# Kernel tuning notes

Measured on AMD Instinct MI355X. Metric: run time of the kernel, lower is better.

## Reference

```python
import jax, jax.numpy as jnp
import numpy as np
import math

B, N, E, H, MLP_H = 4, 1024, 768, 12, 1536
D = E // H
EPS = 1e-6


def clayernorm(x, gamma, beta):
    # x: [..., E, 2]
    real, imag = x[..., 0], x[..., 1]
    mag = jnp.sqrt(real * real + imag * imag + EPS)
    mean = jnp.mean(mag, axis=-1, keepdims=True)
    var = jnp.mean((mag - mean) ** 2, axis=-1, keepdims=True)
    scale = ((mag - mean) / jnp.sqrt(var + EPS)) / (mag + EPS)
    out_r = gamma[:, 0] * (real * scale) + beta[:, 0]
    out_i = gamma[:, 1] * (imag * scale) + beta[:, 1]
    return jnp.stack([out_r, out_i], axis=-1)


def clinear(x, wr, wi, br, bi):
    # x: [..., in, 2]; wr/wi: [out, in]
    xr, xi = x[..., 0], x[..., 1]
    out_r = xr @ wr.T - xi @ wi.T + br
    out_i = xr @ wi.T + xi @ wr.T + bi
    return jnp.stack([out_r, out_i], axis=-1)


def cgelu(x):
    return jnp.stack([jax.nn.gelu(x[..., 0], approximate=False),
                      jax.nn.gelu(x[..., 1], approximate=False)], axis=-1)


def setup_inputs() -> dict:
    key = jax.random.key(0)
    ks = jax.random.split(key, 8)
    std_qkv = math.sqrt(2.0 / (E + 3 * E))
    std_proj = math.sqrt(2.0 / (E + E))
    std_m1 = math.sqrt(2.0 / (E + MLP_H))
    std_m2 = math.sqrt(2.0 / (MLP_H + E))
    return {
        "x": jax.random.normal(ks[0], (B, N, 2 * E), dtype=jnp.float32),
        "g1": jnp.ones((E, 2), jnp.float32), "b1": jnp.zeros((E, 2), jnp.float32),
        "g2": jnp.ones((E, 2), jnp.float32), "b2": jnp.zeros((E, 2), jnp.float32),
        "qkv_wr": std_qkv * jax.random.normal(ks[1], (3 * E, E), jnp.float32),
        "qkv_wi": std_qkv * jax.random.normal(ks[2], (3 * E, E), jnp.float32),
        "qkv_br": jnp.zeros((3 * E,), jnp.float32), "qkv_bi": jnp.zeros((3 * E,), jnp.float32),
        "proj_wr": std_proj * jax.random.normal(ks[3], (E, E), jnp.float32),
        "proj_wi": std_proj * jax.random.normal(ks[4], (E, E), jnp.float32),
        "proj_br": jnp.zeros((E,), jnp.float32), "proj_bi": jnp.zeros((E,), jnp.float32),
        "m1_wr": std_m1 * jax.random.normal(ks[5], (MLP_H, E), jnp.float32),
        "m1_wi": std_m1 * jax.random.normal(ks[6], (MLP_H, E), jnp.float32),
        "m1_br": jnp.zeros((MLP_H,), jnp.float32), "m1_bi": jnp.zeros((MLP_H,), jnp.float32),
        "m2_wr": std_m2 * jax.random.normal(ks[7], (E, MLP_H), jnp.float32),
        "m2_wi": std_m2 * jax.random.normal(jax.random.fold_in(key, 9), (E, MLP_H), jnp.float32),
        "m2_br": jnp.zeros((E,), jnp.float32), "m2_bi": jnp.zeros((E,), jnp.float32),
    }


def _forward(x, g1, b1, g2, b2, qkv_wr, qkv_wi, qkv_br, qkv_bi,
             proj_wr, proj_wi, proj_br, proj_bi,
             m1_wr, m1_wi, m1_br, m1_bi, m2_wr, m2_wi, m2_br, m2_bi):
    xc = x.reshape(B, N, E, 2)
    xn = clayernorm(xc, g1, b1)
    qkv = clinear(xn, qkv_wr, qkv_wi, qkv_br, qkv_bi)      # [B,N,3E,2]
    qkv = qkv.reshape(B, N, 3, H, D, 2).transpose(2, 0, 3, 1, 4, 5)  # [3,B,H,N,D,2]
    q, k, v = qkv[0], qkv[1], qkv[2]
    qr, qi = q[..., 0], q[..., 1]
    kr, ki = k[..., 0], k[..., 1]
    attn_r = jnp.einsum('bhqd,bhkd->bhqk', qr, kr) + jnp.einsum('bhqd,bhkd->bhqk', qi, ki)
    attn_i = jnp.einsum('bhqd,bhkd->bhqk', qr, ki) - jnp.einsum('bhqd,bhkd->bhqk', qi, kr)
    mag = jnp.sqrt(attn_r * attn_r + attn_i * attn_i + 1e-8) / math.sqrt(D)
    w = jax.nn.softmax(mag, axis=-1)
    out_r = jnp.einsum('bhqk,bhkd->bhqd', w, v[..., 0])
    out_i = jnp.einsum('bhqk,bhkd->bhqd', w, v[..., 1])
    attn_out = jnp.stack([out_r, out_i], axis=-1)           # [B,H,N,D,2]
    attn_out = attn_out.transpose(0, 2, 1, 3, 4).reshape(B, N, E, 2)
    attn_out = clinear(attn_out, proj_wr, proj_wi, proj_br, proj_bi)
    xc = xc + attn_out
    xn2 = clayernorm(xc, g2, b2)
    h = clinear(xn2, m1_wr, m1_wi, m1_br, m1_bi)
    h = cgelu(h)
    mlp_out = clinear(h, m2_wr, m2_wi, m2_br, m2_bi)
    xc = xc + mlp_out
    return xc.reshape(B, N, 2 * E)


def reference(x, g1, b1, g2, b2, qkv_wr, qkv_wi, qkv_br, qkv_bi,
              proj_wr, proj_wi, proj_br, proj_bi,
              m1_wr, m1_wi, m1_br, m1_bi, m2_wr, m2_wi, m2_br, m2_bi):
    return _forward(x, g1, b1, g2, b2, qkv_wr, qkv_wi, qkv_br, qkv_bi,
                    proj_wr, proj_wi, proj_br, proj_bi,
                    m1_wr, m1_wi, m1_br, m1_bi, m2_wr, m2_wi, m2_br, m2_bi)
```

## Files before the change

### kernel.cpp

```cpp
#include <hip/hip_runtime.h>
#include <math.h>

#define BB 4
#define NN 1024
#define EE 768
#define HH 12
#define DD 64
#define MLPH 1536
#define RR (BB*NN)
#define SZH ((size_t)48*1024*64)

constexpr float EPS = 1e-6f;

typedef __bf16 bf16_t;
typedef bf16_t bf16x8 __attribute__((ext_vector_type(8)));
typedef bf16_t bf16x4 __attribute__((ext_vector_type(4)));
typedef float  f32x4  __attribute__((ext_vector_type(4)));
typedef unsigned short us8 __attribute__((ext_vector_type(8)));

__device__ __forceinline__ float gelu_exact(float x){
  return 0.5f * x * (1.0f + erff(x * 0.70710678118654752440f));
}

__device__ __forceinline__ bf16x8 negv(bf16x8 v){
  us8 u = __builtin_bit_cast(us8, v);
  u ^= (unsigned short)0x8000;
  return __builtin_bit_cast(bf16x8, u);
}

__device__ __forceinline__ void cvtstore(bf16_t* hp, bf16_t* lp, f32x4 v){
  bf16x4 h, l;
  #pragma unroll
  for (int i=0;i<4;i++){
    float f = v[i];
    bf16_t hb = (bf16_t)f;
    h[i] = hb;
    l[i] = (bf16_t)(f - (float)hb);
  }
  *(bf16x4*)hp = h;
  *(bf16x4*)lp = l;
}

__global__ __launch_bounds__(256) void cln_kernel(
    const float* __restrict__ inI,
    const float* __restrict__ inR, const float* __restrict__ inIm,
    const float* __restrict__ gamma, const float* __restrict__ beta,
    float* __restrict__ outR, float* __restrict__ outI, int mode)
{
  int row = blockIdx.x;
  int t = threadIdx.x;
  __shared__ float sbuf[4];
  float vr[3], vi[3], mg[3];
  #pragma unroll
  for (int j=0;j<3;j++){
    int e = t + 256*j;
    float a, b;
    if (mode == 0){
      a = inI[(size_t)row*(2*EE) + 2*e];
      b = inI[(size_t)row*(2*EE) + 2*e + 1];
    } else {
      a = inR[(size_t)row*EE + e];
      b = inIm[(size_t)row*EE + e];
    }
    vr[j]=a; vi[j]=b;
    mg[j] = sqrtf(a*a + b*b + EPS);
  }
  int lane = t & 63, wv = t >> 6;
  float s = mg[0]+mg[1]+mg[2];
  #pragma unroll
  for (int o=32;o>0;o>>=1) s += __shfl_down(s, o, 64);
  if (lane==0) sbuf[wv] = s;
  __syncthreads();
  float mean = (sbuf[0]+sbuf[1]+sbuf[2]+sbuf[3]) * (1.0f/EE);
  __syncthreads();
  float v = 0.f;
  #pragma unroll
  for (int j=0;j<3;j++){ float d = mg[j]-mean; v += d*d; }
  #pragma unroll
  for (int o=32;o>0;o>>=1) v += __shfl_down(v, o, 64);
  if (lane==0) sbuf[wv] = v;
  __syncthreads();
  float var = (sbuf[0]+sbuf[1]+sbuf[2]+sbuf[3]) * (1.0f/EE);
  float inv = 1.0f / sqrtf(var + EPS);
  #pragma unroll
  for (int j=0;j<3;j++){
    int e = t + 256*j;
    float scale = ((mg[j]-mean) * inv) / (mg[j] + EPS);
    outR[(size_t)row*EE + e] = gamma[2*e]   * (vr[j]*scale) + beta[2*e];
    outI[(size_t)row*EE + e] = gamma[2*e+1] * (vi[j]*scale) + beta[2*e+1];
  }
}

template<int ACT, int RES_MODE, int OUT_MODE>
__global__ __launch_bounds__(256) void cgemm_mfma(
    const float* __restrict__ xr, const float* __restrict__ xi,
    const float* __restrict__ wr, const float* __restrict__ wi,
    const float* __restrict__ br_, const float* __restrict__ bi_,
    const float* __restrict__ resr, const float* __restrict__ resi,
    float* __restrict__ outr, float* __restrict__ outi,
    bf16_t* __restrict__ qsplit,
    int K, int OUT)
{
  __shared__ bf16_t Arh[128][40], Arl[128][40], Aih[128][40], Ail[128][40];
  __shared__ bf16_t Brh[64][40],  Brl[64][40],  Bih[64][40],  Bil[64][40];

  const int tid = threadIdx.x;
  const int rowBase = blockIdx.y * 128, colBase = blockIdx.x * 64;

  const int sr = tid >> 3;
  const int sc = (tid & 7) * 4;

  const int wid = tid >> 6, lane = tid & 63;
  const int wr0 = (wid >> 1) * 64, wc0 = (wid & 1) * 32;
  const int fr = lane & 15, fq = lane >> 4;

  f32x4 accR[4][2], accI[4][2];
  #pragma unroll
  for (int mi=0;mi<4;mi++)
    #pragma unroll
    for (int ni=0;ni<2;ni++){ accR[mi][ni] = (f32x4)0.f; accI[mi][ni] = (f32x4)0.f; }

  f32x4 pAr[4], pAi[4], pBr[2], pBi[2];

  auto LOAD = [&](int k0){
    #pragma unroll
    for (int it=0; it<4; it++){
      const size_t ro = (size_t)(rowBase + sr + it*32)*K + k0 + sc;
      pAr[it] = *(const f32x4*)(xr + ro);
      pAi[it] = *(const f32x4*)(xi + ro);
    }
    #pragma unroll
    for (int it=0; it<2; it++){
      const size_t ro = (size_t)(colBase + sr + it*32)*K + k0 + sc;
      pBr[it] = *(const f32x4*)(wr + ro);
      pBi[it] = *(const f32x4*)(wi + ro);
    }
  };

  LOAD(0);

  for (int k0 = 0; k0 < K; k0 += 32){
    __syncthreads();
    #pragma unroll
    for (int it=0; it<4; it++){
      int r = sr + it*32;
      cvtstore(&Arh[r][sc], &Arl[r][sc], pAr[it]);
      cvtstore(&Aih[r][sc], &Ail[r][sc], pAi[it]);
    }
    #pragma unroll
    for (int it=0; it<2; it++){
      int r = sr + it*32;
      cvtstore(&Brh[r][sc], &Brl[r][sc], pBr[it]);
      cvtstore(&Bih[r][sc], &Bil[r][sc], pBi[it]);
    }
    __syncthreads();
    if (k0 + 32 < K) LOAD(k0 + 32);

    bf16x8 brh[2], brl[2], bih[2], bil[2];
    #pragma unroll
    for (int ni=0; ni<2; ni++){
      int c = wc0 + ni*16 + fr;
      brh[ni] = *(const bf16x8*)&Brh[c][fq*8];
      brl[ni] = *(const bf16x8*)&Brl[c][fq*8];
      bih[ni] = *(const bf16x8*)&Bih[c][fq*8];
      bil[ni] = *(const bf16x8*)&Bil[c][fq*8];
    }
    #pragma unroll
    for (int mi=0; mi<4; mi++){
      int r = wr0 + mi*16 + fr;
      bf16x8 arh = *(const bf16x8*)&Arh[r][fq*8];
      bf16x8 arl = *(const bf16x8*)&Arl[r][fq*8];
      bf16x8 aih = *(const bf16x8*)&Aih[r][fq*8];
      bf16x8 ail = *(const bf16x8*)&Ail[r][fq*8];
      bf16x8 nih = negv(aih), nil_ = negv(ail);
      #pragma unroll
      for (int ni=0; ni<2; ni++){
        f32x4 cR = accR[mi][ni], cI = accI[mi][ni];
        cR = __builtin_amdgcn_mfma_f32_16x16x32_bf16(arh, brh[ni], cR, 0,0,0);
        cR = __builtin_amdgcn_mfma_f32_16x16x32_bf16(arh, brl[ni], cR, 0,0,0);
        cR = __builtin_amdgcn_mfma_f32_16x16x32_bf16(arl, brh[ni], cR, 0,0,0);
        cR = __builtin_amdgcn_mfma_f32_16x16x32_bf16(nih, bih[ni], cR, 0,0,0);
        cR = __builtin_amdgcn_mfma_f32_16x16x32_bf16(nih, bil[ni], cR, 0,0,0);
        cR = __builtin_amdgcn_mfma_f32_16x16x32_bf16(nil_, bih[ni], cR, 0,0,0);
        cI = __builtin_amdgcn_mfma_f32_16x16x32_bf16(arh, bih[ni], cI, 0,0,0);
        cI = __builtin_amdgcn_mfma_f32_16x16x32_bf16(arh, bil[ni], cI, 0,0,0);
        cI = __builtin_amdgcn_mfma_f32_16x16x32_bf16(arl, bih[ni], cI, 0,0,0);
        cI = __builtin_amdgcn_mfma_f32_16x16x32_bf16(aih, brh[ni], cI, 0,0,0);
        cI = __builtin_amdgcn_mfma_f32_16x16x32_bf16(aih, brl[ni], cI, 0,0,0);
        cI = __builtin_amdgcn_mfma_f32_16x16x32_bf16(ail, brh[ni], cI, 0,0,0);
        accR[mi][ni] = cR; accI[mi][ni] = cI;
      }
    }
  }

  #pragma unroll
  for (int mi=0; mi<4; mi++){
    #pragma unroll
    for (int ni=0; ni<2; ni++){
      #pragma unroll
      for (int j=0; j<4; j++){
        int r = rowBase + wr0 + mi*16 + fq*4 + j;
        int c = colBase + wc0 + ni*16 + fr;
        float oR = accR[mi][ni][j] + br_[c];
        float oI = accI[mi][ni][j] + bi_[c];
        if (ACT == 1){ oR = gelu_exact(oR); oI = gelu_exact(oI); }
        if (RES_MODE == 1){
          oR += resr[(size_t)r*OUT + c];
          oI += resi[(size_t)r*OUT + c];
        } else if (RES_MODE == 2){
          oR += resr[(size_t)r*(2*OUT) + 2*c];
          oI += resr[(size_t)r*(2*OUT) + 2*c + 1];
        }
        if (OUT_MODE == 0){
          outr[(size_t)r*OUT + c] = oR;
          outi[(size_t)r*OUT + c] = oI;
        } else if (OUT_MODE == 1){
          outr[(size_t)r*(2*OUT) + 2*c]     = oR;
          outr[(size_t)r*(2*OUT) + 2*c + 1] = oI;
        } else {
          int part = c / EE; int win = c - part*EE;
          int hh = win >> 6, dd = win & 63;
          int bq = r >> 10, nq = r & 1023;
          int bhh = bq*HH + hh;
          size_t idx = (part < 2) ? (((size_t)bhh*NN + nq)*DD + dd)
                                  : (((size_t)bhh*DD + dd)*NN + nq);
          bf16_t* bas = qsplit + (size_t)part*4*SZH;
          bf16_t hR = (bf16_t)oR; bf16_t lR2 = (bf16_t)(oR - (float)hR);
          bf16_t hI = (bf16_t)oI; bf16_t lI2 = (bf16_t)(oI - (float)hI);
          bas[idx]         = hR;
          bas[SZH + idx]   = lR2;
          bas[2*SZH + idx] = hI;
          bas[3*SZH + idx] = lI2;
        }
      }
    }
  }
}

__global__ __launch_bounds__(256) void cattn_mfma(
    const bf16_t* __restrict__ qs,
    float* __restrict__ aor, float* __restrict__ aoi)
{
  __shared__ bf16_t Krh[32][72], Krl[32][72], Kih[32][72], Kil[32][72];
  __shared__ bf16_t Vrh[64][40], Vrl[64][40], Vih[64][40], Vil[64][40];
  __shared__ bf16_t Pl[4][16][40];

  const int tid = threadIdx.x;
  const int lane = tid & 63, wid = tid >> 6;
  const int fr = lane & 15, fq = lane >> 4;
  const int qt = blockIdx.x, bh = blockIdx.y;
  const int b = bh / HH, h = bh - b*HH;

  const bf16_t* Qb = qs;
  const bf16_t* Kb = qs + 4*SZH;
  const bf16_t* Vb = qs + 8*SZH;

  const int qrow = qt*64 + wid*16 + fr;
  bf16x8 q_rh[2], q_rl[2], q_ih[2], q_il[2], nq_ih[2], nq_il[2];
  #pragma unroll
  for (int c=0;c<2;c++){
    size_t o = ((size_t)bh*NN + qrow)*DD + c*32 + fq*8;
    q_rh[c] = *(const bf16x8*)(Qb + 0*SZH + o);
    q_rl[c] = *(const bf16x8*)(Qb + 1*SZH + o);
    q_ih[c] = *(const bf16x8*)(Qb + 2*SZH + o);
    q_il[c] = *(const bf16x8*)(Qb + 3*SZH + o);
    nq_ih[c] = negv(q_ih[c]);
    nq_il[c] = negv(q_il[c]);
  }

  f32x4 accOr[4], accOi[4];
  #pragma unroll
  for (int df=0;df<4;df++){ accOr[df] = (f32x4)0.f; accOi[df] = (f32x4)0.f; }
  float m[4] = {0.f,0.f,0.f,0.f}, l[4] = {0.f,0.f,0.f,0.f};

  const int skr = tid >> 3, skc = (tid & 7) * 8;
  const int svr = tid >> 2, svc = (tid & 3) * 8;

  for (int kt = 0; kt < NN/32; kt++){
    __syncthreads();
    {
      size_t kb = ((size_t)bh*NN + kt*32 + skr)*DD + skc;
      *(bf16x8*)&Krh[skr][skc] = *(const bf16x8*)(Kb + 0*SZH + kb);
      *(bf16x8*)&Krl[skr][skc] = *(const bf16x8*)(Kb + 1*SZH + kb);
      *(bf16x8*)&Kih[skr][skc] = *(const bf16x8*)(Kb + 2*SZH + kb);
      *(bf16x8*)&Kil[skr][skc] = *(const bf16x8*)(Kb + 3*SZH + kb);
      size_t vb = ((size_t)bh*DD + svr)*NN + kt*32 + svc;
      *(bf16x8*)&Vrh[svr][svc] = *(const bf16x8*)(Vb + 0*SZH + vb);
      *(bf16x8*)&Vrl[svr][svc] = *(const bf16x8*)(Vb + 1*SZH + vb);
      *(bf16x8*)&Vih[svr][svc] = *(const bf16x8*)(Vb + 2*SZH + vb);
      *(bf16x8*)&Vil[svr][svc] = *(const bf16x8*)(Vb + 3*SZH + vb);
    }
    __syncthreads();

    f32x4 sr[2], si[2];
    #pragma unroll
    for (int f=0; f<2; f++){
      f32x4 r = (f32x4)0.f, im = (f32x4)0.f;
      #pragma unroll
      for (int c=0; c<2; c++){
        const int kr_ = f*16 + fr, co = c*32 + fq*8;
        bf16x8 krh = *(const bf16x8*)&Krh[kr_][co];
        bf16x8 krl = *(const bf16x8*)&Krl[kr_][co];
        bf16x8 kih = *(const bf16x8*)&Kih[kr_][co];
        bf16x8 kil = *(const bf16x8*)&Kil[kr_][co];
        r = __builtin_amdgcn_mfma_f32_16x16x32_bf16(q_rh[c], krh, r, 0,0,0);
        r = __builtin_amdgcn_mfma_f32_16x16x32_bf16(q_rh[c], krl, r, 0,0,0);
        r = __builtin_amdgcn_mfma_f32_16x16x32_bf16(q_rl[c], krh, r, 0,0,0);
        r = __builtin_amdgcn_mfma_f32_16x16x32_bf16(q_ih[c], kih, r, 0,0,0);
        r = __builtin_amdgcn_mfma_f32_16x16x32_bf16(q_ih[c], kil, r, 0,0,0);
        r = __builtin_amdgcn_mfma_f32_16x16x32_bf16(q_il[c], kih, r, 0,0,0);
        im = __builtin_amdgcn_mfma_f32_16x16x32_bf16(q_rh[c], kih, im, 0,0,0);
        im = __builtin_amdgcn_mfma_f32_16x16x32_bf16(q_rh[c], kil, im, 0,0,0);
        im = __builtin_amdgcn_mfma_f32_16x16x32_bf16(q_rl[c], kih, im, 0,0,0);
        im = __builtin_amdgcn_mfma_f32_16x16x32_bf16(nq_ih[c], krh, im, 0,0,0);
        im = __builtin_amdgcn_mfma_f32_16x16x32_bf16(nq_ih[c], krl, im, 0,0,0);
        im = __builtin_amdgcn_mfma_f32_16x16x32_bf16(nq_il[c], krh, im, 0,0,0);
      }
      sr[f] = r; si[f] = im;
    }

    float mg[2][4];
    #pragma unroll
    for (int f=0; f<2; f++)
      #pragma unroll
      for (int j=0; j<4; j++){
        float a = sr[f][j], c2 = si[f][j];
        mg[f][j] = sqrtf(fmaf(a,a, fmaf(c2,c2, 1e-8f))) * 0.125f;
      }
    float al[4];
    #pragma unroll
    for (int j=0; j<4; j++){
      float mx = fmaxf(mg[0][j], mg[1][j]);
      mx = fmaxf(mx, __shfl_xor(mx, 1, 64));
      mx = fmaxf(mx, __shfl_xor(mx, 2, 64));
      mx = fmaxf(mx, __shfl_xor(mx, 4, 64));
      mx = fmaxf(mx, __shfl_xor(mx, 8, 64));
      float nm = fmaxf(m[j], mx);
      al[j] = __expf(m[j] - nm);
      m[j] = nm;
    }
    unsigned pk[4]; float psum[4];
    #pragma unroll
    for (int j=0; j<4; j++){
      float p0 = __expf(mg[0][j] - m[j]);
      float p1 = __expf(mg[1][j] - m[j]);
      bf16_t b0 = (bf16_t)p0, b1 = (bf16_t)p1;
      pk[j] = (unsigned)__builtin_bit_cast(unsigned short, b0)
            | ((unsigned)__builtin_bit_cast(unsigned short, b1) << 16);
      psum[j] = (float)b0 + (float)b1;
    }
    #pragma unroll
    for (int j=0; j<4; j++){
      float s = psum[j];
      s += __shfl_xor(s, 1, 64);
      s += __shfl_xor(s, 2, 64);
      s += __shfl_xor(s, 4, 64);
      s += __shfl_xor(s, 8, 64);
      l[j] = l[j]*al[j] + s;
      #pragma unroll
      for (int df=0; df<4; df++){ accOr[df][j] *= al[j]; accOi[df][j] *= al[j]; }
    }
    #pragma unroll
    for (int j=0; j<4; j++){
      unsigned partner = (unsigned)__shfl_xor((int)pk[j], 1, 64);
      unsigned word; int kcol;
      if ((fr & 1) == 0){
        word = (pk[j] & 0xFFFFu) | (partner << 16);
        kcol = fr;
      } else {
        word = (partner >> 16) | (pk[j] & 0xFFFF0000u);
        kcol = 15 + fr;
      }
      int q = fq*4 + j;
      *(unsigned*)&Pl[wid][q][kcol] = word;
    }
    __syncthreads();

    bf16x8 pa = *(const bf16x8*)&Pl[wid][fr][fq*8];
    #pragma unroll
    for (int df=0; df<4; df++){
      const int dr = df*16 + fr, co = fq*8;
      bf16x8 vrh = *(const bf16x8*)&Vrh[dr][co];
      bf16x8 vrl = *(const bf16x8*)&Vrl[dr][co];
      bf16x8 vih = *(const bf16x8*)&Vih[dr][co];
      bf16x8 vil = *(const bf16x8*)&Vil[dr][co];
      f32x4 cr = accOr[df], ci = accOi[df];
      cr = __builtin_amdgcn_mfma_f32_16x16x32_bf16(pa, vrh, cr, 0,0,0);
      cr = __builtin_amdgcn_mfma_f32_16x16x32_bf16(pa, vrl, cr, 0,0,0);
      ci = __builtin_amdgcn_mfma_f32_16x16x32_bf16(pa, vih, ci, 0,0,0);
      ci = __builtin_amdgcn_mfma_f32_16x16x32_bf16(pa, vil, ci, 0,0,0);
      accOr[df] = cr; accOi[df] = ci;
    }
  }

  #pragma unroll
  for (int j=0; j<4; j++){
    float invl = 1.0f / l[j];
    size_t r = (size_t)b*NN + qt*64 + wid*16 + fq*4 + j;
    #pragma unroll
    for (int df=0; df<4; df++){
      int col = h*DD + df*16 + fr;
      aor[r*EE + col] = accOr[df][j] * invl;
      aoi[r*EE + col] = accOi[df][j] * invl;
    }
  }
}

extern "C" void kernel_launch(void* const* d_in, const int* in_sizes, int n_in,
                              void* d_out, int out_size, void* d_ws, size_t ws_size,
                              hipStream_t stream) {
  const float* x       = (const float*)d_in[0];
  const float* g1      = (const float*)d_in[1];
  const float* b1      = (const float*)d_in[2];
  const float* g2      = (const float*)d_in[3];
  const float* b2      = (const float*)d_in[4];
  const float* qkv_wr  = (const float*)d_in[5];
  const float* qkv_wi  = (const float*)d_in[6];
  const float* qkv_br  = (const float*)d_in[7];
  const float* qkv_bi  = (const float*)d_in[8];
  const float* proj_wr = (const float*)d_in[9];
  const float* proj_wi = (const float*)d_in[10];
  const float* proj_br = (const float*)d_in[11];
  const float* proj_bi = (const float*)d_in[12];
  const float* m1_wr   = (const float*)d_in[13];
  const float* m1_wi   = (const float*)d_in[14];
  const float* m1_br   = (const float*)d_in[15];
  const float* m1_bi   = (const float*)d_in[16];
  const float* m2_wr   = (const float*)d_in[17];
  const float* m2_wi   = (const float*)d_in[18];
  const float* m2_br   = (const float*)d_in[19];
  const float* m2_bi   = (const float*)d_in[20];

  float* ws = (float*)d_ws;
  const size_t RE = (size_t)RR * EE;
  float* xn_r  = ws;            float* xn_i  = ws + RE;
  float* ao_r  = ws;            float* ao_i  = ws + RE;
  bf16_t* qsplit = (bf16_t*)(ws + 2*RE);
  float* xn2_r = ws + 2*RE;     float* xn2_i = ws + 3*RE;
  float* h_r   = ws + 4*RE;     float* h_i   = ws + 6*RE;
  float* x1_r  = ws + 8*RE;     float* x1_i  = ws + 9*RE;

  cln_kernel<<<RR, 256, 0, stream>>>(x, nullptr, nullptr, g1, b1, xn_r, xn_i, 0);
  cgemm_mfma<0,0,2><<<dim3(36,32), 256, 0, stream>>>(
      xn_r, xn_i, qkv_wr, qkv_wi, qkv_br, qkv_bi,
      nullptr, nullptr, nullptr, nullptr, qsplit, EE, 3*EE);
  cattn_mfma<<<dim3(16,48), 256, 0, stream>>>(qsplit, ao_r, ao_i);
  cgemm_mfma<0,2,0><<<dim3(12,32), 256, 0, stream>>>(
      ao_r, ao_i, proj_wr, proj_wi, proj_br, proj_bi,
      x, nullptr, x1_r, x1_i, nullptr, EE, EE);
  cln_kernel<<<RR, 256, 0, stream>>>(nullptr, x1_r, x1_i, g2, b2, xn2_r, xn2_i, 1);
  cgemm_mfma<1,0,0><<<dim3(24,32), 256, 0, stream>>>(
      xn2_r, xn2_i, m1_wr, m1_wi, m1_br, m1_bi,
      nullptr, nullptr, h_r, h_i, nullptr, EE, MLPH);
  cgemm_mfma<0,1,1><<<dim3(12,32), 256, 0, stream>>>(
      h_r, h_i, m2_wr, m2_wi, m2_br, m2_bi,
      x1_r, x1_i, (float*)d_out, nullptr, nullptr, MLPH, EE);
}
```

Before: 903.3 us.

## Pre-split activations into tiled bf16 hi/lo panels and use 32x32 MFMA GEMM

```diff
diff --git a/kernel.cpp b/kernel.cpp
--- a/kernel.cpp
+++ b/kernel.cpp
@@ -16,7 +16,11 @@
 typedef bf16_t bf16x8 __attribute__((ext_vector_type(8)));
 typedef bf16_t bf16x4 __attribute__((ext_vector_type(4)));
 typedef float  f32x4  __attribute__((ext_vector_type(4)));
+typedef float  f32x16 __attribute__((ext_vector_type(16)));
 typedef unsigned short us8 __attribute__((ext_vector_type(8)));
+
+#define MFMA32 __builtin_amdgcn_mfma_f32_32x32x16_bf16
+#define MFMA16 __builtin_amdgcn_mfma_f32_16x16x32_bf16
 
 __device__ __forceinline__ float gelu_exact(float x){
   return 0.5f * x * (1.0f + erff(x * 0.70710678118654752440f));
@@ -26,6 +30,10 @@
   us8 u = __builtin_bit_cast(us8, v);
   u ^= (unsigned short)0x8000;
   return __builtin_bit_cast(bf16x8, u);
+}
+
+__device__ __forceinline__ void split2(float f, bf16_t& h, bf16_t& l){
+  h = (bf16_t)f; l = (bf16_t)(f - (float)h);
 }
 
 __device__ __forceinline__ void cvtstore(bf16_t* hp, bf16_t* lp, f32x4 v){
@@ -41,12 +49,23 @@
   *(bf16x4*)lp = l;
 }
 
+__device__ __forceinline__ void gload_lds16(const bf16_t* g, bf16_t* l){
+  __builtin_amdgcn_global_load_lds(
+      (const __attribute__((address_space(1))) void*)g,
+      (__attribute__((address_space(3))) void*)l, 16, 0, 0);
+}
+
+__device__ __forceinline__ size_t tiled_ad(int r, int c, int Ko){
+  return (((size_t)(r>>4)*Ko + (c>>3))*16 + (r&15))*8 + (c&7);
+}
+
 __global__ __launch_bounds__(256) void cln_kernel(
     const float* __restrict__ inI,
     const float* __restrict__ inR, const float* __restrict__ inIm,
     const float* __restrict__ gamma, const float* __restrict__ beta,
-    float* __restrict__ outR, float* __restrict__ outI, int mode)
+    bf16_t* __restrict__ out4, int mode)
 {
+  const size_t PS = (size_t)RR*EE;
   int row = blockIdx.x;
   int t = threadIdx.x;
   __shared__ float sbuf[4];
@@ -86,123 +105,138 @@
   for (int j=0;j<3;j++){
     int e = t + 256*j;
     float scale = ((mg[j]-mean) * inv) / (mg[j] + EPS);
-    outR[(size_t)row*EE + e] = gamma[2*e]   * (vr[j]*scale) + beta[2*e];
-    outI[(size_t)row*EE + e] = gamma[2*e+1] * (vi[j]*scale) + beta[2*e+1];
+    float oR = gamma[2*e]   * (vr[j]*scale) + beta[2*e];
+    float oI = gamma[2*e+1] * (vi[j]*scale) + beta[2*e+1];
+    bf16_t hR,lR,hI,lI;
+    split2(oR,hR,lR); split2(oI,hI,lI);
+    size_t ad = tiled_ad(row, e, 96);
+    out4[ad]        = hR;
+    out4[PS + ad]   = lR;
+    out4[2*PS + ad] = hI;
+    out4[3*PS + ad] = lI;
   }
 }
 
 template<int ACT, int RES_MODE, int OUT_MODE>
-__global__ __launch_bounds__(256) void cgemm_mfma(
-    const float* __restrict__ xr, const float* __restrict__ xi,
+__global__ __launch_bounds__(256, 2) void cgemm_v2(
+    const bf16_t* __restrict__ a4,
     const float* __restrict__ wr, const float* __restrict__ wi,
     const float* __restrict__ br_, const float* __restrict__ bi_,
     const float* __restrict__ resr, const float* __restrict__ resi,
     float* __restrict__ outr, float* __restrict__ outi,
-    bf16_t* __restrict__ qsplit,
+    bf16_t* __restrict__ osplit,
     int K, int OUT)
 {
-  __shared__ bf16_t Arh[128][40], Arl[128][40], Aih[128][40], Ail[128][40];
-  __shared__ bf16_t Brh[64][40],  Brl[64][40],  Bih[64][40],  Bil[64][40];
+  __shared__ bf16_t Al[16384];
+  __shared__ bf16_t Bl[16384];
 
   const int tid = threadIdx.x;
-  const int rowBase = blockIdx.y * 128, colBase = blockIdx.x * 64;
-
-  const int sr = tid >> 3;
-  const int sc = (tid & 7) * 4;
-
   const int wid = tid >> 6, lane = tid & 63;
-  const int wr0 = (wid >> 1) * 64, wc0 = (wid & 1) * 32;
-  const int fr = lane & 15, fq = lane >> 4;
-
-  f32x4 accR[4][2], accI[4][2];
-  #pragma unroll
-  for (int mi=0;mi<4;mi++)
-    #pragma unroll
-    for (int ni=0;ni<2;ni++){ accR[mi][ni] = (f32x4)0.f; accI[mi][ni] = (f32x4)0.f; }
-
-  f32x4 pAr[4], pAi[4], pBr[2], pBi[2];
-
-  auto LOAD = [&](int k0){
+  const int rowBase = blockIdx.y * 128, colBase = blockIdx.x * 128;
+  const int Ko = K >> 3;
+  const size_t AS = (size_t)RR * K;
+
+  const int b_so = (tid >> 4) & 3;
+  const int b_se = (tid & 1) * 4;
+  const int b_r0 = ((tid & 15) >> 1) + 8*wid;
+
+  const int fr2 = lane & 31, fq2 = lane >> 5;
+  const int wr0 = (wid >> 1) * 64, wc0 = (wid & 1) * 64;
+
+  f32x16 accR[2][2], accI[2][2];
+  #pragma unroll
+  for (int mi=0;mi<2;mi++)
+    #pragma unroll
+    for (int ni=0;ni<2;ni++){ accR[mi][ni] = (f32x16)0.f; accI[mi][ni] = (f32x16)0.f; }
+
+  f32x4 pBr[4], pBi[4];
+  auto LOADB = [&](int k0){
     #pragma unroll
     for (int it=0; it<4; it++){
-      const size_t ro = (size_t)(rowBase + sr + it*32)*K + k0 + sc;
-      pAr[it] = *(const f32x4*)(xr + ro);
-      pAi[it] = *(const f32x4*)(xi + ro);
-    }
-    #pragma unroll
-    for (int it=0; it<2; it++){
-      const size_t ro = (size_t)(colBase + sr + it*32)*K + k0 + sc;
+      size_t ro = (size_t)(colBase + b_r0 + it*32)*K + k0 + b_so*8 + b_se;
       pBr[it] = *(const f32x4*)(wr + ro);
       pBi[it] = *(const f32x4*)(wi + ro);
     }
   };
-
-  LOAD(0);
+  LOADB(0);
 
   for (int k0 = 0; k0 < K; k0 += 32){
+    const int o0 = k0 >> 3;
     __syncthreads();
     #pragma unroll
     for (int it=0; it<4; it++){
-      int r = sr + it*32;
-      cvtstore(&Arh[r][sc], &Arl[r][sc], pAr[it]);
-      cvtstore(&Aih[r][sc], &Ail[r][sc], pAi[it]);
-    }
-    #pragma unroll
-    for (int it=0; it<2; it++){
-      int r = sr + it*32;
-      cvtstore(&Brh[r][sc], &Brl[r][sc], pBr[it]);
-      cvtstore(&Bih[r][sc], &Bil[r][sc], pBi[it]);
+      int r = b_r0 + it*32;
+      int off = ((r>>4)*4 + b_so)*128 + (r&15)*8 + b_se;
+      cvtstore(&Bl[off],       &Bl[4096+off],  pBr[it]);
+      cvtstore(&Bl[8192+off],  &Bl[12288+off], pBi[it]);
+    }
+    #pragma unroll
+    for (int q=0; q<4; q++){
+      #pragma unroll
+      for (int s2=0; s2<2; s2++){
+        int pi = wid*2 + s2;
+        const bf16_t* g = a4 + (size_t)q*AS
+            + ((size_t)(blockIdx.y*8 + pi)*Ko + o0)*128 + lane*8;
+        gload_lds16(g, &Al[q*4096 + pi*512]);
+      }
     }
     __syncthreads();
-    if (k0 + 32 < K) LOAD(k0 + 32);
-
-    bf16x8 brh[2], brl[2], bih[2], bil[2];
+    if (k0 + 32 < K) LOADB(k0 + 32);
+
+    #pragma unroll
+    for (int ks=0; ks<2; ks++){
+      bf16x8 brh[2], brl[2], bih[2], bil[2];
+      #pragma unroll
+      for (int ni=0; ni<2; ni++){
+        int panelB = (wid&1)*4 + ni*2 + (fr2>>4);
+        int off = ((panelB*4 + ks*2 + fq2)*16 + (fr2&15))*8;
+        brh[ni] = *(const bf16x8*)&Bl[off];
+        brl[ni] = *(const bf16x8*)&Bl[4096+off];
+        bih[ni] = *(const bf16x8*)&Bl[8192+off];
+        bil[ni] = *(const bf16x8*)&Bl[12288+off];
+      }
+      #pragma unroll
+      for (int mi=0; mi<2; mi++){
+        int panelA = (wid>>1)*4 + mi*2 + (fr2>>4);
+        int off = ((panelA*4 + ks*2 + fq2)*16 + (fr2&15))*8;
+        bf16x8 arh = *(const bf16x8*)&Al[off];
+        bf16x8 arl = *(const bf16x8*)&Al[4096+off];
+        bf16x8 aih = *(const bf16x8*)&Al[8192+off];
+        bf16x8 ail = *(const bf16x8*)&Al[12288+off];
+        bf16x8 nih = negv(aih), nil_ = negv(ail);
+        #pragma unroll
+        for (int ni=0; ni<2; ni++){
+          f32x16 cR = accR[mi][ni], cI = accI[mi][ni];
+          cR = MFMA32(arh,  brh[ni], cR, 0,0,0);
+          cR = MFMA32(arh,  brl[ni], cR, 0,0,0);
+          cR = MFMA32(arl,  brh[ni], cR, 0,0,0);
+          cR = MFMA32(nih,  bih[ni], cR, 0,0,0);
+          cR = MFMA32(nih,  bil[ni], cR, 0,0,0);
+          cR = MFMA32(nil_, bih[ni], cR, 0,0,0);
+          cI = MFMA32(arh,  bih[ni], cI, 0,0,0);
+          cI = MFMA32(arh,  bil[ni], cI, 0,0,0);
+          cI = MFMA32(arl,  bih[ni], cI, 0,0,0);
+          cI = MFMA32(aih,  brh[ni], cI, 0,0,0);
+          cI = MFMA32(aih,  brl[ni], cI, 0,0,0);
+          cI = MFMA32(ail,  brh[ni], cI, 0,0,0);
+          accR[mi][ni] = cR; accI[mi][ni] = cI;
+        }
+      }
+    }
+  }
+
+  const size_t OS = (size_t)RR * OUT;
+  #pragma unroll
+  for (int mi=0; mi<2; mi++){
     #pragma unroll
     for (int ni=0; ni<2; ni++){
-      int c = wc0 + ni*16 + fr;
-      brh[ni] = *(const bf16x8*)&Brh[c][fq*8];
-      brl[ni] = *(const bf16x8*)&Brl[c][fq*8];
-      bih[ni] = *(const bf16x8*)&Bih[c][fq*8];
-      bil[ni] = *(const bf16x8*)&Bil[c][fq*8];
-    }
-    #pragma unroll
-    for (int mi=0; mi<4; mi++){
-      int r = wr0 + mi*16 + fr;
-      bf16x8 arh = *(const bf16x8*)&Arh[r][fq*8];
-      bf16x8 arl = *(const bf16x8*)&Arl[r][fq*8];
-      bf16x8 aih = *(const bf16x8*)&Aih[r][fq*8];
-      bf16x8 ail = *(const bf16x8*)&Ail[r][fq*8];
-      bf16x8 nih = negv(aih), nil_ = negv(ail);
-      #pragma unroll
-      for (int ni=0; ni<2; ni++){
-        f32x4 cR = accR[mi][ni], cI = accI[mi][ni];
-        cR = __builtin_amdgcn_mfma_f32_16x16x32_bf16(arh, brh[ni], cR, 0,0,0);
-        cR = __builtin_amdgcn_mfma_f32_16x16x32_bf16(arh, brl[ni], cR, 0,0,0);
-        cR = __builtin_amdgcn_mfma_f32_16x16x32_bf16(arl, brh[ni], cR, 0,0,0);
-        cR = __builtin_amdgcn_mfma_f32_16x16x32_bf16(nih, bih[ni], cR, 0,0,0);
-        cR = __builtin_amdgcn_mfma_f32_16x16x32_bf16(nih, bil[ni], cR, 0,0,0);
-        cR = __builtin_amdgcn_mfma_f32_16x16x32_bf16(nil_, bih[ni], cR, 0,0,0);
-        cI = __builtin_amdgcn_mfma_f32_16x16x32_bf16(arh, bih[ni], cI, 0,0,0);
-        cI = __builtin_amdgcn_mfma_f32_16x16x32_bf16(arh, bil[ni], cI, 0,0,0);
-        cI = __builtin_amdgcn_mfma_f32_16x16x32_bf16(arl, bih[ni], cI, 0,0,0);
-        cI = __builtin_amdgcn_mfma_f32_16x16x32_bf16(aih, brh[ni], cI, 0,0,0);
-        cI = __builtin_amdgcn_mfma_f32_16x16x32_bf16(aih, brl[ni], cI, 0,0,0);
-        cI = __builtin_amdgcn_mfma_f32_16x16x32_bf16(ail, brh[ni], cI, 0,0,0);
-        accR[mi][ni] = cR; accI[mi][ni] = cI;
-      }
-    }
-  }
-
-  #pragma unroll
-  for (int mi=0; mi<4; mi++){
-    #pragma unroll
-    for (int ni=0; ni<2; ni++){
-      #pragma unroll
-      for (int j=0; j<4; j++){
-        int r = rowBase + wr0 + mi*16 + fq*4 + j;
-        int c = colBase + wc0 + ni*16 + fr;
-        float oR = accR[mi][ni][j] + br_[c];
-        float oI = accI[mi][ni][j] + bi_[c];
+      int c = colBase + wc0 + ni*32 + fr2;
+      float bR = br_[c], bI = bi_[c];
+      #pragma unroll
+      for (int j=0; j<16; j++){
+        int r = rowBase + wr0 + mi*32 + (j&3) + 8*(j>>2) + 4*fq2;
+        float oR = accR[mi][ni][j] + bR;
+        float oI = accI[mi][ni][j] + bI;
         if (ACT == 1){ oR = gelu_exact(oR); oI = gelu_exact(oI); }
         if (RES_MODE == 1){
           oR += resr[(size_t)r*OUT + c];
@@ -217,20 +251,28 @@
         } else if (OUT_MODE == 1){
           outr[(size_t)r*(2*OUT) + 2*c]     = oR;
           outr[(size_t)r*(2*OUT) + 2*c + 1] = oI;
-        } else {
+        } else if (OUT_MODE == 2){
           int part = c / EE; int win = c - part*EE;
           int hh = win >> 6, dd = win & 63;
           int bq = r >> 10, nq = r & 1023;
           int bhh = bq*HH + hh;
           size_t idx = (part < 2) ? (((size_t)bhh*NN + nq)*DD + dd)
                                   : (((size_t)bhh*DD + dd)*NN + nq);
-          bf16_t* bas = qsplit + (size_t)part*4*SZH;
-          bf16_t hR = (bf16_t)oR; bf16_t lR2 = (bf16_t)(oR - (float)hR);
-          bf16_t hI = (bf16_t)oI; bf16_t lI2 = (bf16_t)(oI - (float)hI);
+          bf16_t* bas = osplit + (size_t)part*4*SZH;
+          bf16_t hR,lR,hI,lI;
+          split2(oR,hR,lR); split2(oI,hI,lI);
           bas[idx]         = hR;
-          bas[SZH + idx]   = lR2;
+          bas[SZH + idx]   = lR;
           bas[2*SZH + idx] = hI;
-          bas[3*SZH + idx] = lI2;
+          bas[3*SZH + idx] = lI;
+        } else {
+          bf16_t hR,lR,hI,lI;
+          split2(oR,hR,lR); split2(oI,hI,lI);
+          size_t ad = tiled_ad(r, c, OUT>>3);
+          osplit[ad]        = hR;
+          osplit[OS + ad]   = lR;
+          osplit[2*OS + ad] = hI;
+          osplit[3*OS + ad] = lI;
         }
       }
     }
@@ -239,7 +281,7 @@
 
 __global__ __launch_bounds__(256) void cattn_mfma(
     const bf16_t* __restrict__ qs,
-    float* __restrict__ aor, float* __restrict__ aoi)
+    bf16_t* __restrict__ ao4)
 {
   __shared__ bf16_t Krh[32][72], Krl[32][72], Kih[32][72], Kil[32][72];
   __shared__ bf16_t Vrh[64][40], Vrl[64][40], Vih[64][40], Vil[64][40];
@@ -303,18 +345,18 @@
         bf16x8 krl = *(const bf16x8*)&Krl[kr_][co];
         bf16x8 kih = *(const bf16x8*)&Kih[kr_][co];
         bf16x8 kil = *(const bf16x8*)&Kil[kr_][co];
-        r = __builtin_amdgcn_mfma_f32_16x16x32_bf16(q_rh[c], krh, r, 0,0,0);
-        r = __builtin_amdgcn_mfma_f32_16x16x32_bf16(q_rh[c], krl, r, 0,0,0);
-        r = __builtin_amdgcn_mfma_f32_16x16x32_bf16(q_rl[c], krh, r, 0,0,0);
-        r = __builtin_amdgcn_mfma_f32_16x16x32_bf16(q_ih[c], kih, r, 0,0,0);
-        r = __builtin_amdgcn_mfma_f32_16x16x32_bf16(q_ih[c], kil, r, 0,0,0);
-        r = __builtin_amdgcn_mfma_f32_16x16x32_bf16(q_il[c], kih, r, 0,0,0);
-        im = __builtin_amdgcn_mfma_f32_16x16x32_bf16(q_rh[c], kih, im, 0,0,0);
-        im = __builtin_amdgcn_mfma_f32_16x16x32_bf16(q_rh[c], kil, im, 0,0,0);
-        im = __builtin_amdgcn_mfma_f32_16x16x32_bf16(q_rl[c], kih, im, 0,0,0);
-        im = __builtin_amdgcn_mfma_f32_16x16x32_bf16(nq_ih[c], krh, im, 0,0,0);
-        im = __builtin_amdgcn_mfma_f32_16x16x32_bf16(nq_ih[c], krl, im, 0,0,0);
-        im = __builtin_amdgcn_mfma_f32_16x16x32_bf16(nq_il[c], krh, im, 0,0,0);
+        r = MFMA16(q_rh[c], krh, r, 0,0,0);
+        r = MFMA16(q_rh[c], krl, r, 0,0,0);
+        r = MFMA16(q_rl[c], krh, r, 0,0,0);
+        r = MFMA16(q_ih[c], kih, r, 0,0,0);
+        r = MFMA16(q_ih[c], kil, r, 0,0,0);
+        r = MFMA16(q_il[c], kih, r, 0,0,0);
+        im = MFMA16(q_rh[c], kih, im, 0,0,0);
+        im = MFMA16(q_rh[c], kil, im, 0,0,0);
+        im = MFMA16(q_rl[c], kih, im, 0,0,0);
+        im = MFMA16(nq_ih[c], krh, im, 0,0,0);
+        im = MFMA16(nq_ih[c], krl, im, 0,0,0);
+        im = MFMA16(nq_il[c], krh, im, 0,0,0);
       }
       sr[f] = r; si[f] = im;
     }
@@ -385,23 +427,31 @@
       bf16x8 vih = *(const bf16x8*)&Vih[dr][co];
       bf16x8 vil = *(const bf16x8*)&Vil[dr][co];
       f32x4 cr = accOr[df], ci = accOi[df];
-      cr = __builtin_amdgcn_mfma_f32_16x16x32_bf16(pa, vrh, cr, 0,0,0);
-      cr = __builtin_amdgcn_mfma_f32_16x16x32_bf16(pa, vrl, cr, 0,0,0);
-      ci = __builtin_amdgcn_mfma_f32_16x16x32_bf16(pa, vih, ci, 0,0,0);
-      ci = __builtin_amdgcn_mfma_f32_16x16x32_bf16(pa, vil, ci, 0,0,0);
+      cr = MFMA16(pa, vrh, cr, 0,0,0);
+      cr = MFMA16(pa, vrl, cr, 0,0,0);
+      ci = MFMA16(pa, vih, ci, 0,0,0);
+      ci = MFMA16(pa, vil, ci, 0,0,0);
       accOr[df] = cr; accOi[df] = ci;
     }
   }
 
+  const size_t PS = (size_t)RR*EE;
   #pragma unroll
   for (int j=0; j<4; j++){
     float invl = 1.0f / l[j];
-    size_t r = (size_t)b*NN + qt*64 + wid*16 + fq*4 + j;
+    int r = b*NN + qt*64 + wid*16 + fq*4 + j;
     #pragma unroll
     for (int df=0; df<4; df++){
-      int col = h*DD + df*16 + fr;
-      aor[r*EE + col] = accOr[df][j] * invl;
-      aoi[r*EE + col] = accOi[df][j] * invl;
+      int c = h*DD + df*16 + fr;
+      float vR = accOr[df][j] * invl;
+      float vI = accOi[df][j] * invl;
+      bf16_t hR,lR,hI,lI;
+      split2(vR,hR,lR); split2(vI,hI,lI);
+      size_t ad = tiled_ad(r, c, 96);
+      ao4[ad]        = hR;
+      ao4[PS + ad]   = lR;
+      ao4[2*PS + ad] = hI;
+      ao4[3*PS + ad] = lI;
     }
   }
 }
@@ -433,26 +483,26 @@
 
   float* ws = (float*)d_ws;
   const size_t RE = (size_t)RR * EE;
-  float* xn_r  = ws;            float* xn_i  = ws + RE;
-  float* ao_r  = ws;            float* ao_i  = ws + RE;
+  bf16_t* xn4 = (bf16_t*)ws;
+  bf16_t* ao4 = (bf16_t*)ws;
   bf16_t* qsplit = (bf16_t*)(ws + 2*RE);
-  float* xn2_r = ws + 2*RE;     float* xn2_i = ws + 3*RE;
-  float* h_r   = ws + 4*RE;     float* h_i   = ws + 6*RE;
+  bf16_t* xn2_4  = (bf16_t*)(ws + 2*RE);
+  bf16_t* h4     = (bf16_t*)(ws + 4*RE);
   float* x1_r  = ws + 8*RE;     float* x1_i  = ws + 9*RE;
 
-  cln_kernel<<<RR, 256, 0, stream>>>(x, nullptr, nullptr, g1, b1, xn_r, xn_i, 0);
-  cgemm_mfma<0,0,2><<<dim3(36,32), 256, 0, stream>>>(
-      xn_r, xn_i, qkv_wr, qkv_wi, qkv_br, qkv_bi,
+  cln_kernel<<<RR, 256, 0, stream>>>(x, nullptr, nullptr, g1, b1, xn4, 0);
+  cgemm_v2<0,0,2><<<dim3(18,32), 256, 0, stream>>>(
+      xn4, qkv_wr, qkv_wi, qkv_br, qkv_bi,
       nullptr, nullptr, nullptr, nullptr, qsplit, EE, 3*EE);
-  cattn_mfma<<<dim3(16,48), 256, 0, stream>>>(qsplit, ao_r, ao_i);
-  cgemm_mfma<0,2,0><<<dim3(12,32), 256, 0, stream>>>(
-      ao_r, ao_i, proj_wr, proj_wi, proj_br, proj_bi,
+  cattn_mfma<<<dim3(16,48), 256, 0, stream>>>(qsplit, ao4);
+  cgemm_v2<0,2,0><<<dim3(6,32), 256, 0, stream>>>(
+      ao4, proj_wr, proj_wi, proj_br, proj_bi,
       x, nullptr, x1_r, x1_i, nullptr, EE, EE);
-  cln_kernel<<<RR, 256, 0, stream>>>(nullptr, x1_r, x1_i, g2, b2, xn2_r, xn2_i, 1);
-  cgemm_mfma<1,0,0><<<dim3(24,32), 256, 0, stream>>>(
-      xn2_r, xn2_i, m1_wr, m1_wi, m1_br, m1_bi,
-      nullptr, nullptr, h_r, h_i, nullptr, EE, MLPH);
-  cgemm_mfma<0,1,1><<<dim3(12,32), 256, 0, stream>>>(
-      h_r, h_i, m2_wr, m2_wi, m2_br, m2_bi,
+  cln_kernel<<<RR, 256, 0, stream>>>(nullptr, x1_r, x1_i, g2, b2, xn2_4, 1);
+  cgemm_v2<1,0,3><<<dim3(12,32), 256, 0, stream>>>(
+      xn2_4, m1_wr, m1_wi, m1_br, m1_bi,
+      nullptr, nullptr, nullptr, nullptr, h4, EE, MLPH);
+  cgemm_v2<0,1,1><<<dim3(6,32), 256, 0, stream>>>(
+      h4, m2_wr, m2_wi, m2_br, m2_bi,
       x1_r, x1_i, (float*)d_out, nullptr, nullptr, MLPH, EE);
 }
```

Measured after the change: 1.169 ms. +29.4%, slower.
